# Optimization experiments

Hardware: AMD Instinct MI355X
Metric: run time of the kernel (lower is better)

The kernel has to match this reference:

```python
import jax, jax.numpy as jnp
import numpy as np

CELU_ALPHA = 3.0  # hardcoded in the torch module (nn.CELU(alpha=3.0), F.celu(alpha=3.0))

def celu(x):
    # celu(x, a) = max(0, x) + min(0, a*(exp(x/a)-1)); overflow-safe form
    return jnp.maximum(x, 0.0) + CELU_ALPHA * jnp.expm1(jnp.minimum(x, 0.0) / CELU_ALPHA)

def setup_inputs() -> dict:
    key = jax.random.key(0)
    k1, k2, k3, k4, k5 = jax.random.split(key, 5)
    N, E, H, D = 16384, 262144, 4, 64
    return {
        "features": jax.random.normal(k1, (N, D), dtype=jnp.float32),
        "metapath_embedding": jax.random.normal(k2, (E, D), dtype=jnp.float32),
        "attn1_w": jax.random.normal(k3, (H, D), dtype=jnp.float32) * 0.15,  # xavier-ish scale
        "attn2": jax.random.normal(k4, (H, D), dtype=jnp.float32) * 0.15,
        "segment_ids": jax.random.randint(k5, (E,), 0, N, dtype=jnp.int32),
    }

def reference(features, metapath_embedding, attn1_w, attn2, segment_ids):
    N, D = features.shape
    H = attn1_w.shape[0]
    # eft: same embedding broadcast over heads (torch.cat([emb]*H).view(-1,H,D))
    eft = celu(metapath_embedding)                    # [E, D]
    a1 = celu(features @ attn1_w.T)                   # [N, H] (per-node, shared across its instances)
    a2 = eft @ attn2.T                                # [E, H]
    a = celu(a1[segment_ids] + a2)                    # [E, H]
    # segment softmax over instances of each node
    m = jax.lax.stop_gradient(jax.ops.segment_max(a, segment_ids, num_segments=N))  # [N, H]
    ex = jnp.exp(a - m[segment_ids])                  # [E, H]
    denom = jax.ops.segment_sum(ex, segment_ids, num_segments=N)                    # [N, H]
    att = ex / denom[segment_ids]                     # [E, H]
    # weighted sum of eft over each node's instances -> [N, H, D]
    msg = jax.ops.segment_sum(att[:, :, None] * eft[:, None, :], segment_ids, num_segments=N)
    # empty segments yield 0 and celu(0)=0, matching the torch zero-fill branch
    return celu(msg).reshape(N, H * D)
```

## Files before the change

### kernel.cpp

```cpp
#include <hip/hip_runtime.h>
#include <math.h>

#define CAP 64

__device__ __forceinline__ float celu3(float x) {
    return fmaxf(x, 0.0f) + 3.0f * (__expf(fminf(x, 0.0f) * (1.0f / 3.0f)) - 1.0f);
}

template <int CTRL>
__device__ __forceinline__ float dpp_add(float v) {
    int o = __builtin_amdgcn_update_dpp(0, __float_as_int(v), CTRL, 0xf, 0xf, true);
    return v + __int_as_float(o);
}
__device__ __forceinline__ float red16(float v) {
    v = dpp_add<0xB1>(v);
    v = dpp_add<0x4E>(v);
    v = dpp_add<0x124>(v);
    v = dpp_add<0x128>(v);
    return v;
}
__device__ __forceinline__ float wave_sum64(float v) {
    v = red16(v);
    v += __shfl_xor(v, 16, 64);
    v += __shfl_xor(v, 32, 64);
    return v;
}


__global__ __launch_bounds__(256) void init_kernel(
    int* __restrict__ counts, int N,
    const float* __restrict__ feat, const float* __restrict__ w1,
    float* __restrict__ a1)
{
    int nblk_zero = (N + 255) / 256;
    if ((int)blockIdx.x < nblk_zero) {
        int i = blockIdx.x * 256 + threadIdx.x;
        if (i < N) counts[i] = 0;
        return;
    }
    int n = (blockIdx.x - nblk_zero) * 4 + (threadIdx.x >> 6);
    int lane = threadIdx.x & 63;
    if (n >= N) return;
    float f = feat[(long)n * 64 + lane];
    float s[4];
#pragma unroll
    for (int h = 0; h < 4; ++h) s[h] = wave_sum64(f * w1[h * 64 + lane]);
    if (lane < 4) a1[n * 4 + lane] = celu3(s[lane]);
}


__global__ __launch_bounds__(256) void hist_kernel(
    const int* __restrict__ seg, int* __restrict__ counts,
    int* __restrict__ elist, int E)
{
    int i = blockIdx.x * 256 + threadIdx.x;
    int stride = gridDim.x * 256;
    for (; i < E; i += stride) {
        int s = seg[i];
        int r = atomicAdd(&counts[s], 1);
        if (r < CAP) elist[s * CAP + r] = i;
    }
}


__global__ __launch_bounds__(256) void fused_kernel(
    const float* __restrict__ meta, const float* __restrict__ w2,
    const float* __restrict__ a1, const int* __restrict__ counts,
    const int* __restrict__ elist, const int* __restrict__ seg,
    float* __restrict__ out, int N, int E)
{
    int t = threadIdx.x;
    int lane = t & 63;
    int wv = t >> 6;
    int n = blockIdx.x * 4 + wv;
    if (n >= N) return;

    int cnt = counts[n];
    int g = lane >> 4;
    int q = lane & 15;
    long ob = (long)n * 256 + g * 64 + q * 4;

    if (cnt == 0) {
        float4 z = {0.f, 0.f, 0.f, 0.f};
        *(float4*)(out + ob) = z;
        return;
    }

    float4 a1v = *(const float4*)(a1 + (long)n * 4);

    if (cnt <= CAP) {
        float4 w2q0 = *(const float4*)(w2 + 0 * 64 + q * 4);
        float4 w2q1 = *(const float4*)(w2 + 1 * 64 + q * 4);
        float4 w2q2 = *(const float4*)(w2 + 2 * 64 + q * 4);
        float4 w2q3 = *(const float4*)(w2 + 3 * 64 + q * 4);

        int eid_l = (lane < cnt) ? elist[n * CAP + lane] : 0;

        float sp0 = 0.f, sp1 = 0.f, sp2 = 0.f, sp3 = 0.f;
        float4 acc0 = {0,0,0,0}, acc1 = {0,0,0,0}, acc2 = {0,0,0,0}, acc3 = {0,0,0,0};

        int nch = (cnt + 3) >> 2;
#pragma unroll 4
        for (int c = 0; c < nch; ++c) {
            int j = c * 4 + g;
            bool vr = j < cnt;
            int eid = __shfl(eid_l, j);
            float4 v = *(const float4*)(meta + (long)eid * 64 + q * 4);
            float4 ef;
            ef.x = celu3(v.x); ef.y = celu3(v.y); ef.z = celu3(v.z); ef.w = celu3(v.w);

            float d0 = ef.x * w2q0.x + ef.y * w2q0.y + ef.z * w2q0.z + ef.w * w2q0.w;
            float d1 = ef.x * w2q1.x + ef.y * w2q1.y + ef.z * w2q1.z + ef.w * w2q1.w;
            float d2 = ef.x * w2q2.x + ef.y * w2q2.y + ef.z * w2q2.z + ef.w * w2q2.w;
            float d3 = ef.x * w2q3.x + ef.y * w2q3.y + ef.z * w2q3.z + ef.w * w2q3.w;
            d0 = red16(d0); d1 = red16(d1); d2 = red16(d2); d3 = red16(d3);

            float A0 = vr ? celu3(a1v.x + d0) : -INFINITY;
            float A1 = vr ? celu3(a1v.y + d1) : -INFINITY;
            float A2 = vr ? celu3(a1v.z + d2) : -INFINITY;
            float A3 = vr ? celu3(a1v.w + d3) : -INFINITY;

            float p0 = __expf(fminf(A0, 80.f));
            float p1 = __expf(fminf(A1, 80.f));
            float p2 = __expf(fminf(A2, 80.f));
            float p3 = __expf(fminf(A3, 80.f));

            sp0 += p0; sp1 += p1; sp2 += p2; sp3 += p3;

            acc0.x = fmaf(p0, ef.x, acc0.x); acc0.y = fmaf(p0, ef.y, acc0.y);
            acc0.z = fmaf(p0, ef.z, acc0.z); acc0.w = fmaf(p0, ef.w, acc0.w);
            acc1.x = fmaf(p1, ef.x, acc1.x); acc1.y = fmaf(p1, ef.y, acc1.y);
            acc1.z = fmaf(p1, ef.z, acc1.z); acc1.w = fmaf(p1, ef.w, acc1.w);
            acc2.x = fmaf(p2, ef.x, acc2.x); acc2.y = fmaf(p2, ef.y, acc2.y);
            acc2.z = fmaf(p2, ef.z, acc2.z); acc2.w = fmaf(p2, ef.w, acc2.w);
            acc3.x = fmaf(p3, ef.x, acc3.x); acc3.y = fmaf(p3, ef.y, acc3.y);
            acc3.z = fmaf(p3, ef.z, acc3.z); acc3.w = fmaf(p3, ef.w, acc3.w);
        }

        sp0 += __shfl_xor(sp0, 16); sp0 += __shfl_xor(sp0, 32);
        sp1 += __shfl_xor(sp1, 16); sp1 += __shfl_xor(sp1, 32);
        sp2 += __shfl_xor(sp2, 16); sp2 += __shfl_xor(sp2, 32);
        sp3 += __shfl_xor(sp3, 16); sp3 += __shfl_xor(sp3, 32);

        acc0.x += __shfl_xor(acc0.x, 16); acc0.x += __shfl_xor(acc0.x, 32);
        acc0.y += __shfl_xor(acc0.y, 16); acc0.y += __shfl_xor(acc0.y, 32);
        acc0.z += __shfl_xor(acc0.z, 16); acc0.z += __shfl_xor(acc0.z, 32);
        acc0.w += __shfl_xor(acc0.w, 16); acc0.w += __shfl_xor(acc0.w, 32);
        acc1.x += __shfl_xor(acc1.x, 16); acc1.x += __shfl_xor(acc1.x, 32);
        acc1.y += __shfl_xor(acc1.y, 16); acc1.y += __shfl_xor(acc1.y, 32);
        acc1.z += __shfl_xor(acc1.z, 16); acc1.z += __shfl_xor(acc1.z, 32);
        acc1.w += __shfl_xor(acc1.w, 16); acc1.w += __shfl_xor(acc1.w, 32);
        acc2.x += __shfl_xor(acc2.x, 16); acc2.x += __shfl_xor(acc2.x, 32);
        acc2.y += __shfl_xor(acc2.y, 16); acc2.y += __shfl_xor(acc2.y, 32);
        acc2.z += __shfl_xor(acc2.z, 16); acc2.z += __shfl_xor(acc2.z, 32);
        acc2.w += __shfl_xor(acc2.w, 16); acc2.w += __shfl_xor(acc2.w, 32);
        acc3.x += __shfl_xor(acc3.x, 16); acc3.x += __shfl_xor(acc3.x, 32);
        acc3.y += __shfl_xor(acc3.y, 16); acc3.y += __shfl_xor(acc3.y, 32);
        acc3.z += __shfl_xor(acc3.z, 16); acc3.z += __shfl_xor(acc3.z, 32);
        acc3.w += __shfl_xor(acc3.w, 16); acc3.w += __shfl_xor(acc3.w, 32);

        float rs0 = 1.f / sp0, rs1 = 1.f / sp1, rs2 = 1.f / sp2, rs3 = 1.f / sp3;

        float4 av = (g == 0) ? acc0 : (g == 1) ? acc1 : (g == 2) ? acc2 : acc3;
        float rg = (g == 0) ? rs0 : (g == 1) ? rs1 : (g == 2) ? rs2 : rs3;
        float4 o;
        o.x = celu3(av.x * rg); o.y = celu3(av.y * rg);
        o.z = celu3(av.z * rg); o.w = celu3(av.w * rg);
        *(float4*)(out + ob) = o;
        return;
    }

    {
        float a10 = a1v.x, a11 = a1v.y, a12 = a1v.z, a13 = a1v.w;
        float w2v0 = w2[0 * 64 + lane], w2v1 = w2[1 * 64 + lane];
        float w2v2 = w2[2 * 64 + lane], w2v3 = w2[3 * 64 + lane];
        float m0 = -INFINITY, m1 = -INFINITY, m2 = -INFINITY, m3 = -INFINITY;
        float s0 = 0.f, s1 = 0.f, s2 = 0.f, s3 = 0.f;
        float ac0 = 0.f, ac1 = 0.f, ac2 = 0.f, ac3 = 0.f;
        for (int base = 0; base < E; base += 64) {
            int e = base + lane;
            bool hit = (e < E) && (seg[e] == n);
            unsigned long long ball = __ballot(hit);
            while (ball) {
                int b = __ffsll((long long)ball) - 1;
                ball &= ball - 1;
                int eid = base + b;
                float eft = celu3(meta[(long)eid * 64 + lane]);
                float d0 = wave_sum64(eft * w2v0);
                float d1 = wave_sum64(eft * w2v1);
                float d2 = wave_sum64(eft * w2v2);
                float d3 = wave_sum64(eft * w2v3);
                float A0 = celu3(a10 + d0), A1 = celu3(a11 + d1);
                float A2 = celu3(a12 + d2), A3 = celu3(a13 + d3);
                float nm0 = fmaxf(m0, A0), nm1 = fmaxf(m1, A1);
                float nm2 = fmaxf(m2, A2), nm3 = fmaxf(m3, A3);
                float al0 = __expf(m0 - nm0), al1 = __expf(m1 - nm1);
                float al2 = __expf(m2 - nm2), al3 = __expf(m3 - nm3);
                float p0 = __expf(A0 - nm0), p1 = __expf(A1 - nm1);
                float p2 = __expf(A2 - nm2), p3 = __expf(A3 - nm3);
                s0 = fmaf(al0, s0, p0); s1 = fmaf(al1, s1, p1);
                s2 = fmaf(al2, s2, p2); s3 = fmaf(al3, s3, p3);
                ac0 = fmaf(p0, eft, al0 * ac0); ac1 = fmaf(p1, eft, al1 * ac1);
                ac2 = fmaf(p2, eft, al2 * ac2); ac3 = fmaf(p3, eft, al3 * ac3);
                m0 = nm0; m1 = nm1; m2 = nm2; m3 = nm3;
            }
        }
        long ob2 = (long)n * 256 + lane;
        out[ob2]       = celu3(ac0 / s0);
        out[ob2 + 64]  = celu3(ac1 / s1);
        out[ob2 + 128] = celu3(ac2 / s2);
        out[ob2 + 192] = celu3(ac3 / s3);
    }
}


extern "C" void kernel_launch(void* const* d_in, const int* in_sizes, int n_in,
                              void* d_out, int out_size, void* d_ws, size_t ws_size,
                              hipStream_t stream)
{
    const float* feat = (const float*)d_in[0];
    const float* meta = (const float*)d_in[1];
    const float* w1   = (const float*)d_in[2];
    const float* w2   = (const float*)d_in[3];
    const int*   seg  = (const int*)d_in[4];
    float* out = (float*)d_out;

    int N = in_sizes[0] / 64;
    int E = in_sizes[4];

    float* a1   = (float*)d_ws;
    int* counts = (int*)(a1 + (size_t)N * 4);
    int* elist  = counts + N;

    int nblk_zero = (N + 255) / 256;
    int nblk_a1   = (N + 3) / 4;

    init_kernel<<<nblk_zero + nblk_a1, 256, 0, stream>>>(counts, N, feat, w1, a1);
    hist_kernel<<<512, 256, 0, stream>>>(seg, counts, elist, E);
    fused_kernel<<<(N + 3) / 4, 256, 0, stream>>>(meta, w2, a1, counts, elist, seg, out, N, E);
}
```

Baseline: 48.67 us.

## Pad per-node counters, fuse histogram with a1 computation, load edge ids directly

Per-node atomic counters are padded to a 64-byte stride so concurrent atomics from different nodes land on separate cache lines. The histogram pass is merged with the per-node attention (a1) computation into one launch with 1024 histogram blocks, and zeroing moves to its own small kernel. In the fused kernel, edge ids are now read straight from the edge list on each chunk instead of being loaded once and broadcast with a shuffle. The cost is a 16x larger counter array to zero, possible contention between the merged workloads, and more scattered global loads of edge ids.

Result: slower. 52.29 us (+7.4%).

```diff
diff --git a/kernel.cpp b/kernel.cpp
--- a/kernel.cpp
+++ b/kernel.cpp
@@ -2,6 +2,7 @@
 #include <math.h>
 
 #define CAP 64
+#define CSTRIDE 16
 
 __device__ __forceinline__ float celu3(float x) {
     return fmaxf(x, 0.0f) + 3.0f * (__expf(fminf(x, 0.0f) * (1.0f / 3.0f)) - 1.0f);
@@ -27,18 +28,29 @@
 }
 
 
-__global__ __launch_bounds__(256) void init_kernel(
-    int* __restrict__ counts, int N,
+__global__ __launch_bounds__(256) void zero_kernel(int* __restrict__ p, int n) {
+    int i = blockIdx.x * 256 + threadIdx.x;
+    if (i < n) p[i] = 0;
+}
+
+
+__global__ __launch_bounds__(256) void hist_a1_kernel(
+    const int* __restrict__ seg, int* __restrict__ counts, int* __restrict__ elist, int E,
     const float* __restrict__ feat, const float* __restrict__ w1,
-    float* __restrict__ a1)
+    float* __restrict__ a1, int N)
 {
-    int nblk_zero = (N + 255) / 256;
-    if ((int)blockIdx.x < nblk_zero) {
+    const int NHIST = 1024;
+    if ((int)blockIdx.x < NHIST) {
         int i = blockIdx.x * 256 + threadIdx.x;
-        if (i < N) counts[i] = 0;
+        int stride = NHIST * 256;
+        for (; i < E; i += stride) {
+            int s = seg[i];
+            int r = atomicAdd(&counts[s * CSTRIDE], 1);
+            if (r < CAP) elist[s * CAP + r] = i;
+        }
         return;
     }
-    int n = (blockIdx.x - nblk_zero) * 4 + (threadIdx.x >> 6);
+    int n = (blockIdx.x - NHIST) * 4 + (threadIdx.x >> 6);
     int lane = threadIdx.x & 63;
     if (n >= N) return;
     float f = feat[(long)n * 64 + lane];
@@ -46,20 +58,6 @@
 #pragma unroll
     for (int h = 0; h < 4; ++h) s[h] = wave_sum64(f * w1[h * 64 + lane]);
     if (lane < 4) a1[n * 4 + lane] = celu3(s[lane]);
-}
-
-
-__global__ __launch_bounds__(256) void hist_kernel(
-    const int* __restrict__ seg, int* __restrict__ counts,
-    int* __restrict__ elist, int E)
-{
-    int i = blockIdx.x * 256 + threadIdx.x;
-    int stride = gridDim.x * 256;
-    for (; i < E; i += stride) {
-        int s = seg[i];
-        int r = atomicAdd(&counts[s], 1);
-        if (r < CAP) elist[s * CAP + r] = i;
-    }
 }
 
 
@@ -75,7 +73,7 @@
     int n = blockIdx.x * 4 + wv;
     if (n >= N) return;
 
-    int cnt = counts[n];
+    int cnt = counts[n * CSTRIDE];
     int g = lane >> 4;
     int q = lane & 15;
     long ob = (long)n * 256 + g * 64 + q * 4;
@@ -94,7 +92,7 @@
         float4 w2q2 = *(const float4*)(w2 + 2 * 64 + q * 4);
         float4 w2q3 = *(const float4*)(w2 + 3 * 64 + q * 4);
 
-        int eid_l = (lane < cnt) ? elist[n * CAP + lane] : 0;
+        const int* el = elist + (long)n * CAP;
 
         float sp0 = 0.f, sp1 = 0.f, sp2 = 0.f, sp3 = 0.f;
         float4 acc0 = {0,0,0,0}, acc1 = {0,0,0,0}, acc2 = {0,0,0,0}, acc3 = {0,0,0,0};
@@ -104,7 +102,7 @@
         for (int c = 0; c < nch; ++c) {
             int j = c * 4 + g;
             bool vr = j < cnt;
-            int eid = __shfl(eid_l, j);
+            int eid = el[vr ? j : 0];
             float4 v = *(const float4*)(meta + (long)eid * 64 + q * 4);
             float4 ef;
             ef.x = celu3(v.x); ef.y = celu3(v.y); ef.z = celu3(v.z); ef.w = celu3(v.w);
@@ -230,12 +228,12 @@
 
     float* a1   = (float*)d_ws;
     int* counts = (int*)(a1 + (size_t)N * 4);
-    int* elist  = counts + N;
-
-    int nblk_zero = (N + 255) / 256;
-    int nblk_a1   = (N + 3) / 4;
-
-    init_kernel<<<nblk_zero + nblk_a1, 256, 0, stream>>>(counts, N, feat, w1, a1);
-    hist_kernel<<<512, 256, 0, stream>>>(seg, counts, elist, E);
+    int* elist  = counts + (size_t)N * CSTRIDE;
+
+    int nz = N * CSTRIDE;
+    int nblk_a1 = (N + 3) / 4;
+
+    zero_kernel<<<(nz + 255) / 256, 256, 0, stream>>>(counts, nz);
+    hist_a1_kernel<<<1024 + nblk_a1, 256, 0, stream>>>(seg, counts, elist, E, feat, w1, a1, N);
     fused_kernel<<<(N + 3) / 4, 256, 0, stream>>>(meta, w2, a1, counts, elist, seg, out, N, E);
 }
```
